# Kernel tuning notes

Hardware: AMD Instinct MI355X
Metric: run time of the kernel (lower is better)

Reference implementation:

```python
import jax, jax.numpy as jnp
import numpy as np

D_MODEL, N_HEADS = 512, 8
HEAD_DIM = D_MODEL // N_HEADS
LN_EPS = 1e-5


def setup_inputs() -> dict:
    key = jax.random.key(0)
    ks = jax.random.split(key, 6)
    b, n = 8, 1024
    x = jax.random.normal(ks[0], (b, n, D_MODEL), dtype=jnp.float32)
    W_qkv = jax.random.normal(ks[1], (D_MODEL, 3 * D_MODEL), dtype=jnp.float32) * (1.0 / np.sqrt(D_MODEL))
    b_qkv = jnp.zeros((3 * D_MODEL,), dtype=jnp.float32)
    reattn_w = jax.random.normal(ks[2], (N_HEADS, N_HEADS), dtype=jnp.float32)
    ln_g = jnp.ones((N_HEADS,), dtype=jnp.float32)
    ln_b = jnp.zeros((N_HEADS,), dtype=jnp.float32)
    W_out = jax.random.normal(ks[3], (D_MODEL, D_MODEL), dtype=jnp.float32) * (1.0 / np.sqrt(D_MODEL))
    b_out = jnp.zeros((D_MODEL,), dtype=jnp.float32)
    return {"x": x, "W_qkv": W_qkv, "b_qkv": b_qkv, "reattn_w": reattn_w,
            "ln_g": ln_g, "ln_b": ln_b, "W_out": W_out, "b_out": b_out}


def reference(x, W_qkv, b_qkv, reattn_w, ln_g, ln_b, W_out, b_out):
    b, n, _ = x.shape
    scale = jnp.float32(HEAD_DIM ** -0.5)  # lsa=False -> non-trainable constant
    qkv = x @ W_qkv + b_qkv                                  # (b, n, 3*d_model)
    q, k, v = jnp.split(qkv, 3, axis=-1)
    def to_heads(t):  # b n (h d) -> b h n d
        return t.reshape(b, n, N_HEADS, HEAD_DIM).transpose(0, 2, 1, 3)
    q, k, v = to_heads(q), to_heads(k), to_heads(v)
    scores = jnp.einsum('bhid,bhjd->bhij', q, k) * scale      # (b, h, n, n)
    attn = jax.nn.softmax(scores, axis=-1)
    # cross-head re-attention mix
    attn = jnp.einsum('bhij,hk->bkij', attn, reattn_w)
    # LayerNorm over the head axis (axis=1)
    mu = jnp.mean(attn, axis=1, keepdims=True)
    var = jnp.var(attn, axis=1, keepdims=True)
    attn = (attn - mu) * jax.lax.rsqrt(var + LN_EPS)
    attn = attn * ln_g[None, :, None, None] + ln_b[None, :, None, None]
    out = jnp.einsum('bhij,bhjd->bhid', attn, v)              # (b, h, n, d)
    out = out.transpose(0, 2, 1, 3).reshape(b, n, D_MODEL)    # b n (h d)
    out = out @ W_out + b_out
    return (out, attn)
```

## Files before the change

### kernel.cpp

```cpp
#include <hip/hip_runtime.h>
#include <hip/hip_bf16.h>

#define SCALE_ 0.125f
#define LN_EPS_ 1e-5f

typedef __attribute__((ext_vector_type(8))) short bf16x8;
typedef __attribute__((ext_vector_type(4))) float f32x4;

__device__ __forceinline__ ushort f2b(float f) {
  union { float f; unsigned u; } x; x.f = f;
  unsigned r = x.u + 0x7FFFu + ((x.u >> 16) & 1u);
  return (ushort)(r >> 16);
}
__device__ __forceinline__ unsigned cvtpk(float lo, float hi) {
  union { __hip_bfloat162 h; unsigned u; } x;
  x.h = __float22bfloat162_rn(make_float2(lo, hi));
  return x.u;
}

__device__ __forceinline__ f32x4 mfma16(bf16x8 a, bf16x8 b, f32x4 c) {
  return __builtin_amdgcn_mfma_f32_16x16x32_bf16(a, b, c, 0, 0, 0);
}

__device__ __forceinline__ void bar_lds() {
  asm volatile("s_waitcnt lgkmcnt(0)\n\ts_barrier" ::: "memory");
  __builtin_amdgcn_sched_barrier(0);
}

__global__ __launch_bounds__(256) void cast_transpose(const float* __restrict__ src,
                                                      ushort* __restrict__ dst,
                                                      int R, int C) {
  __shared__ ushort t[64][65];
  const int tid = threadIdx.x;
  const int c0 = blockIdx.x * 64, r0 = blockIdx.y * 64;
  const int lr = tid >> 2, lc = (tid & 3) * 16;
#pragma unroll
  for (int u = 0; u < 4; ++u) {
    float4 v = *(const float4*)&src[(size_t)(r0 + lr) * C + c0 + lc + u * 4];
    t[lc + u * 4 + 0][lr] = f2b(v.x);
    t[lc + u * 4 + 1][lr] = f2b(v.y);
    t[lc + u * 4 + 2][lr] = f2b(v.z);
    t[lc + u * 4 + 3][lr] = f2b(v.w);
  }
  __syncthreads();
#pragma unroll
  for (int u = 0; u < 2; ++u) {
    bf16x8 o;
#pragma unroll
    for (int e = 0; e < 8; ++e) o[e] = (short)t[lr][lc + u * 8 + e];
    *(bf16x8*)&dst[(size_t)(c0 + lr) * R + r0 + lc + u * 8] = o;
  }
}

__global__ __launch_bounds__(256) void qkv_mfma(const float* __restrict__ x,
                                                const ushort* __restrict__ Wt,
                                                const float* __restrict__ bias,
                                                ushort* __restrict__ q,
                                                ushort* __restrict__ k,
                                                ushort* __restrict__ vt) {
  __shared__ ushort A[128][40];
  __shared__ ushort Bs[128][40];
  const int tid = threadIdx.x;
  const int n0 = blockIdx.x * 128;
  const int m0 = blockIdx.y * 128;
  const int lane = tid & 63, wid = tid >> 6;
  const int wr = wid >> 1, wc = wid & 1;
  const int lr = lane & 15, g4 = lane >> 4;
  const int sr = tid >> 1, sco = (tid & 1) * 16;
  f32x4 acc[4][4] = {};
  for (int k0 = 0; k0 < 512; k0 += 32) {
    {
      const float4* xs = (const float4*)&x[(size_t)(m0 + sr) * 512 + k0 + sco];
      float4 v0 = xs[0], v1 = xs[1], v2 = xs[2], v3 = xs[3];
      bf16x8 p0, p1;
      p0[0] = (short)f2b(v0.x); p0[1] = (short)f2b(v0.y);
      p0[2] = (short)f2b(v0.z); p0[3] = (short)f2b(v0.w);
      p0[4] = (short)f2b(v1.x); p0[5] = (short)f2b(v1.y);
      p0[6] = (short)f2b(v1.z); p0[7] = (short)f2b(v1.w);
      p1[0] = (short)f2b(v2.x); p1[1] = (short)f2b(v2.y);
      p1[2] = (short)f2b(v2.z); p1[3] = (short)f2b(v2.w);
      p1[4] = (short)f2b(v3.x); p1[5] = (short)f2b(v3.y);
      p1[6] = (short)f2b(v3.z); p1[7] = (short)f2b(v3.w);
      *(bf16x8*)&A[sr][sco] = p0;
      *(bf16x8*)&A[sr][sco + 8] = p1;
    }
    {
      const bf16x8* wp = (const bf16x8*)&Wt[(size_t)(n0 + sr) * 512 + k0 + sco];
      *(bf16x8*)&Bs[sr][sco] = wp[0];
      *(bf16x8*)&Bs[sr][sco + 8] = wp[1];
    }
    __syncthreads();
    bf16x8 af[4], bf[4];
#pragma unroll
    for (int mr = 0; mr < 4; ++mr) af[mr] = *(bf16x8*)&A[wr * 64 + mr * 16 + lr][g4 * 8];
#pragma unroll
    for (int nr = 0; nr < 4; ++nr) bf[nr] = *(bf16x8*)&Bs[wc * 64 + nr * 16 + lr][g4 * 8];
#pragma unroll
    for (int mr = 0; mr < 4; ++mr)
#pragma unroll
      for (int nr = 0; nr < 4; ++nr) acc[mr][nr] = mfma16(af[mr], bf[nr], acc[mr][nr]);
    __syncthreads();
  }
  const int part = n0 >> 9;
#pragma unroll
  for (int mr = 0; mr < 4; ++mr)
#pragma unroll
    for (int nr = 0; nr < 4; ++nr) {
      const int n = n0 + wc * 64 + nr * 16 + lr;
      const int h = (n & 511) >> 6, d = n & 63;
      const float bb = bias[n];
#pragma unroll
      for (int r = 0; r < 4; ++r) {
        int token = m0 + wr * 64 + mr * 16 + g4 * 4 + r;
        int bi = token >> 10, ii = token & 1023;
        ushort valb = f2b(acc[mr][nr][r] + bb);
        if (part == 0)
          q[(((size_t)(bi * 8 + h) * 1024 + ii) * 64) + d] = valb;
        else if (part == 1)
          k[(((size_t)(bi * 8 + h) * 1024 + ii) * 64) + d] = valb;
        else
          vt[((size_t)(bi * 8 + h) * 64 + d) * 1024 + ii] = valb;
      }
    }
}

__global__ __launch_bounds__(64) void denoms(const ushort* __restrict__ q,
                                             const ushort* __restrict__ k,
                                             float* __restrict__ invg) {
  const int bid = blockIdx.x;
  const int obid = ((bid & 7) << 8) + (bid >> 3);
  const int bh = obid >> 5;
  const int it = obid & 31;
  const int lane = threadIdx.x;
  const int lr = lane & 15, g4 = lane >> 4;
  const ushort* qh = q + ((size_t)bh * 1024 + it * 32) * 64;
  const ushort* kh = k + (size_t)bh * 65536;

  bf16x8 qf[2][2];
#pragma unroll
  for (int ir = 0; ir < 2; ++ir)
#pragma unroll
    for (int ks = 0; ks < 2; ++ks)
      qf[ir][ks] = *(const bf16x8*)&qh[(size_t)(ir * 16 + lr) * 64 + ks * 32 + g4 * 8];

  float psum[2] = {0.f, 0.f};
  bf16x8 kc[4], kn[4];
#pragma unroll
  for (int jr = 0; jr < 2; ++jr)
#pragma unroll
    for (int ks = 0; ks < 2; ++ks)
      kc[jr * 2 + ks] = *(const bf16x8*)&kh[(size_t)(jr * 16 + lr) * 64 + ks * 32 + g4 * 8];
  for (int jt = 0; jt < 32; ++jt) {
    const int j0n = ((jt + 1) & 31) * 32;
#pragma unroll
    for (int jr = 0; jr < 2; ++jr)
#pragma unroll
      for (int ks = 0; ks < 2; ++ks)
        kn[jr * 2 + ks] =
            *(const bf16x8*)&kh[(size_t)(j0n + jr * 16 + lr) * 64 + ks * 32 + g4 * 8];
    f32x4 sa[2][2] = {};
#pragma unroll
    for (int jr = 0; jr < 2; ++jr)
#pragma unroll
      for (int ir = 0; ir < 2; ++ir) {
        sa[jr][ir] = mfma16(kc[jr * 2 + 0], qf[ir][0], sa[jr][ir]);
        sa[jr][ir] = mfma16(kc[jr * 2 + 1], qf[ir][1], sa[jr][ir]);
      }
#pragma unroll
    for (int jr = 0; jr < 2; ++jr)
#pragma unroll
      for (int ir = 0; ir < 2; ++ir)
#pragma unroll
        for (int r = 0; r < 4; ++r) psum[ir] += __expf(sa[jr][ir][r] * SCALE_);
#pragma unroll
    for (int i = 0; i < 4; ++i) kc[i] = kn[i];
  }
#pragma unroll
  for (int ir = 0; ir < 2; ++ir) {
    float s = psum[ir];
    s += __shfl_xor(s, 16);
    s += __shfl_xor(s, 32);
    psum[ir] = s;
  }
  if (lane < 16) {
    invg[(size_t)bh * 1024 + it * 32 + lr] = 1.0f / psum[0];
    invg[(size_t)bh * 1024 + it * 32 + 16 + lr] = 1.0f / psum[1];
  }
}

__global__ __launch_bounds__(512, 2) void attn_fused(const ushort* __restrict__ q,
                                                     const ushort* __restrict__ k,
                                                     const ushort* __restrict__ vt,
                                                     const float* __restrict__ rw,
                                                     const float* __restrict__ ln_g,
                                                     const float* __restrict__ ln_b,
                                                     const float* __restrict__ invg,
                                                     float* __restrict__ attn,
                                                     ushort* __restrict__ pv) {
  __shared__ float PM[8][32][36];
  __shared__ float wsh[64];
  __shared__ float gsh[8], bsh[8];

  const int tid = threadIdx.x;
  const int lane = tid & 63;
  const int h = tid >> 6;
  const int obid = ((blockIdx.x & 7) << 5) + (blockIdx.x >> 3);
  const int i0 = (obid & 31) * 32;
  const int b = obid >> 5;
  const int lr = lane & 15, g4 = lane >> 4;

  const int bh = b * 8 + h;
  const ushort* qh = q + ((size_t)bh * 1024 + i0) * 64;
  const ushort* kh = k + (size_t)bh * 65536;
  const ushort* vth = vt + (size_t)bh * 65536;

  if (tid < 64) wsh[tid] = rw[tid];
  if (tid < 8) { gsh[tid] = ln_g[tid]; bsh[tid] = ln_b[tid]; }

  bf16x8 qf[2][2];
#pragma unroll
  for (int ir = 0; ir < 2; ++ir)
#pragma unroll
    for (int ks = 0; ks < 2; ++ks)
      qf[ir][ks] = *(const bf16x8*)&qh[(size_t)(ir * 16 + lr) * 64 + ks * 32 + g4 * 8];

  float inv_[2];
#pragma unroll
  for (int ir = 0; ir < 2; ++ir)
    inv_[ir] = invg[(size_t)bh * 1024 + i0 + ir * 16 + lr];

  f32x4 oaccT[4][2] = {};
  const int pair = tid & 1, chunk = tid >> 1;
  const int m_ii = chunk >> 3, m_jj = (chunk & 7) * 4;
  const int k2base = pair * 4;

  bf16x8 kc[4], kn[4];
#pragma unroll
  for (int jr = 0; jr < 2; ++jr)
#pragma unroll
    for (int ks = 0; ks < 2; ++ks)
      kc[jr * 2 + ks] = *(const bf16x8*)&kh[(size_t)(jr * 16 + lr) * 64 + ks * 32 + g4 * 8];

  for (int jt = 0; jt < 32; ++jt) {
    const int j0 = jt * 32;
    const int j0n = ((jt + 1) & 31) * 32;
#pragma unroll
    for (int jr = 0; jr < 2; ++jr)
#pragma unroll
      for (int ks = 0; ks < 2; ++ks)
        kn[jr * 2 + ks] =
            *(const bf16x8*)&kh[(size_t)(j0n + jr * 16 + lr) * 64 + ks * 32 + g4 * 8];

    f32x4 sa[2][2] = {};
#pragma unroll
    for (int jr = 0; jr < 2; ++jr)
#pragma unroll
      for (int ir = 0; ir < 2; ++ir) {
        sa[jr][ir] = mfma16(kc[jr * 2 + 0], qf[ir][0], sa[jr][ir]);
        sa[jr][ir] = mfma16(kc[jr * 2 + 1], qf[ir][1], sa[jr][ir]);
      }
#pragma unroll
    for (int jr = 0; jr < 2; ++jr)
#pragma unroll
      for (int ir = 0; ir < 2; ++ir) {
        f32x4 pw;
#pragma unroll
        for (int r = 0; r < 4; ++r) pw[r] = __expf(sa[jr][ir][r] * SCALE_) * inv_[ir];
        *(f32x4*)&PM[h][ir * 16 + lr][jr * 16 + g4 * 4] = pw;
      }

    bf16x8 vc[4];
#pragma unroll
    for (int dr = 0; dr < 4; ++dr)
      vc[dr] = *(const bf16x8*)&vth[(size_t)(dr * 16 + lr) * 1024 + j0 + g4 * 8];

    bar_lds();

    float4 ph[8];
#pragma unroll
    for (int h2 = 0; h2 < 8; ++h2) ph[h2] = *(const float4*)&PM[h2][m_ii][m_jj];
    float mixed[4][4];
#pragma unroll
    for (int k2l = 0; k2l < 4; ++k2l) {
      float a0 = 0.f, a1 = 0.f, a2 = 0.f, a3 = 0.f;
#pragma unroll
      for (int h2 = 0; h2 < 8; ++h2) {
        float w = wsh[h2 * 8 + k2base + k2l];
        a0 += ph[h2].x * w; a1 += ph[h2].y * w;
        a2 += ph[h2].z * w; a3 += ph[h2].w * w;
      }
      mixed[k2l][0] = a0; mixed[k2l][1] = a1; mixed[k2l][2] = a2; mixed[k2l][3] = a3;
    }
    float mu[4], rs_[4];
#pragma unroll
    for (int e = 0; e < 4; ++e) {
      float mp = mixed[0][e] + mixed[1][e] + mixed[2][e] + mixed[3][e];
      mu[e] = (mp + __shfl_xor(mp, 1)) * 0.125f;
    }
#pragma unroll
    for (int e = 0; e < 4; ++e) {
      float vp = 0.f;
#pragma unroll
      for (int k2l = 0; k2l < 4; ++k2l) {
        float d = mixed[k2l][e] - mu[e];
        vp += d * d;
      }
      float var = (vp + __shfl_xor(vp, 1)) * 0.125f;
      rs_[e] = rsqrtf(var + LN_EPS_);
    }
#pragma unroll
    for (int k2l = 0; k2l < 4; ++k2l) {
      int k2 = k2base + k2l;
      float g = gsh[k2], be = bsh[k2];
      f32x4 o;
      o[0] = (mixed[k2l][0] - mu[0]) * rs_[0] * g + be;
      o[1] = (mixed[k2l][1] - mu[1]) * rs_[1] * g + be;
      o[2] = (mixed[k2l][2] - mu[2]) * rs_[2] * g + be;
      o[3] = (mixed[k2l][3] - mu[3]) * rs_[3] * g + be;
      *(f32x4*)&attn[((size_t)(b * 8 + k2) << 20) + ((size_t)(i0 + m_ii) << 10) +
                     j0 + m_jj] = o;
      *(f32x4*)&PM[k2][m_ii][m_jj] = o;
    }

    bar_lds();

    bf16x8 pab[2];
#pragma unroll
    for (int ic = 0; ic < 2; ++ic) {
      const float* pr = &PM[h][ic * 16 + lr][g4 * 8];
      float4 p0 = *(const float4*)&pr[0];
      float4 p1 = *(const float4*)&pr[4];
      union { bf16x8 v; unsigned u[4]; } pk;
      pk.u[0] = cvtpk(p0.x, p0.y);
      pk.u[1] = cvtpk(p0.z, p0.w);
      pk.u[2] = cvtpk(p1.x, p1.y);
      pk.u[3] = cvtpk(p1.z, p1.w);
      pab[ic] = pk.v;
    }
#pragma unroll
    for (int dr = 0; dr < 4; ++dr) {
      oaccT[dr][0] = mfma16(vc[dr], pab[0], oaccT[dr][0]);
      oaccT[dr][1] = mfma16(vc[dr], pab[1], oaccT[dr][1]);
    }

#pragma unroll
    for (int i = 0; i < 4; ++i) kc[i] = kn[i];
  }

  ushort* po = pv + ((size_t)bh * 1024 + i0) * 64;
#pragma unroll
  for (int ic = 0; ic < 2; ++ic)
#pragma unroll
    for (int dr = 0; dr < 4; ++dr) {
      union { ushort4 s; unsigned u[2]; } o;
      o.u[0] = cvtpk(oaccT[dr][ic][0], oaccT[dr][ic][1]);
      o.u[1] = cvtpk(oaccT[dr][ic][2], oaccT[dr][ic][3]);
      *(ushort4*)&po[(size_t)(ic * 16 + lr) * 64 + dr * 16 + g4 * 4] = o.s;
    }
}

__global__ __launch_bounds__(256) void out_mfma(const ushort* __restrict__ pvb,
                                                const ushort* __restrict__ Wt,
                                                const float* __restrict__ bias,
                                                float* __restrict__ out) {
  __shared__ ushort A[128][40];
  __shared__ ushort Bs[128][40];
  const int tid = threadIdx.x;
  const int n0 = blockIdx.x * 128;
  const int m0 = blockIdx.y * 128;
  const int lane = tid & 63, wid = tid >> 6;
  const int wr = wid >> 1, wc = wid & 1;
  const int lr = lane & 15, g4 = lane >> 4;
  const int sr = tid >> 1, sco = (tid & 1) * 16;
  f32x4 acc[4][4] = {};
  for (int k0 = 0; k0 < 512; k0 += 32) {
    {
      int token = m0 + sr;
      int bi = token >> 10, ii = token & 1023;
      int f = k0 + sco;
      int hh = f >> 6, d = f & 63;
      const bf16x8* src =
          (const bf16x8*)&pvb[(((size_t)(bi * 8 + hh)) * 1024 + ii) * 64 + d];
      *(bf16x8*)&A[sr][sco] = src[0];
      *(bf16x8*)&A[sr][sco + 8] = src[1];
    }
    {
      const bf16x8* wp = (const bf16x8*)&Wt[(size_t)(n0 + sr) * 512 + k0 + sco];
      *(bf16x8*)&Bs[sr][sco] = wp[0];
      *(bf16x8*)&Bs[sr][sco + 8] = wp[1];
    }
    __syncthreads();
    bf16x8 af[4], bf[4];
#pragma unroll
    for (int mr = 0; mr < 4; ++mr) af[mr] = *(bf16x8*)&A[wr * 64 + mr * 16 + lr][g4 * 8];
#pragma unroll
    for (int nr = 0; nr < 4; ++nr) bf[nr] = *(bf16x8*)&Bs[wc * 64 + nr * 16 + lr][g4 * 8];
#pragma unroll
    for (int mr = 0; mr < 4; ++mr)
#pragma unroll
      for (int nr = 0; nr < 4; ++nr) acc[mr][nr] = mfma16(af[mr], bf[nr], acc[mr][nr]);
    __syncthreads();
  }
#pragma unroll
  for (int mr = 0; mr < 4; ++mr)
#pragma unroll
    for (int nr = 0; nr < 4; ++nr) {
      const int n = n0 + wc * 64 + nr * 16 + lr;
      const float bb = bias[n];
#pragma unroll
      for (int r = 0; r < 4; ++r) {
        int token = m0 + wr * 64 + mr * 16 + g4 * 4 + r;
        out[(size_t)token * 512 + n] = acc[mr][nr][r] + bb;
      }
    }
}

extern "C" void kernel_launch(void* const* d_in, const int* in_sizes, int n_in,
                              void* d_out, int out_size, void* d_ws, size_t ws_size,
                              hipStream_t stream) {
  const float* x    = (const float*)d_in[0];
  const float* Wqkv = (const float*)d_in[1];
  const float* bqkv = (const float*)d_in[2];
  const float* rw   = (const float*)d_in[3];
  const float* lng  = (const float*)d_in[4];
  const float* lnb  = (const float*)d_in[5];
  const float* Wout = (const float*)d_in[6];
  const float* bout = (const float*)d_in[7];

  float* out  = (float*)d_out;
  float* attn = (float*)d_out + 4194304;

  char* wsb = (char*)d_ws;
  ushort* q     = (ushort*)(wsb);
  ushort* k     = (ushort*)(wsb + (8u << 20));
  ushort* vt    = (ushort*)(wsb + (16u << 20));
  ushort* pvb   = (ushort*)(wsb + (24u << 20));
  ushort* Wqkvt = (ushort*)(wsb + (32u << 20));
  ushort* Woutt = (ushort*)(wsb + (33u << 20) + (1u << 19));
  float*  invg  = (float*)(wsb + (34u << 20));

  cast_transpose<<<dim3(24, 8), 256, 0, stream>>>(Wqkv, Wqkvt, 512, 1536);
  cast_transpose<<<dim3(8, 8), 256, 0, stream>>>(Wout, Woutt, 512, 512);

  qkv_mfma<<<dim3(12, 64), 256, 0, stream>>>(x, Wqkvt, bqkv, q, k, vt);
  denoms<<<dim3(2048), 64, 0, stream>>>(q, k, invg);
  attn_fused<<<dim3(256), 512, 0, stream>>>(q, k, vt, rw, lng, lnb, invg, attn, pvb);
  out_mfma<<<dim3(4, 64), 256, 0, stream>>>(pvb, Woutt, bout, out);
}
```

Measured before the change: 190.1 us.

## Add dedicated store warps with double-buffered LDS for attn output writes

```diff
diff --git a/kernel.cpp b/kernel.cpp
--- a/kernel.cpp
+++ b/kernel.cpp
@@ -188,7 +188,7 @@
   }
 }
 
-__global__ __launch_bounds__(512, 2) void attn_fused(const ushort* __restrict__ q,
+__global__ __launch_bounds__(768, 2) void attn_fused(const ushort* __restrict__ q,
                                                      const ushort* __restrict__ k,
                                                      const ushort* __restrict__ vt,
                                                      const float* __restrict__ rw,
@@ -197,20 +197,21 @@
                                                      const float* __restrict__ invg,
                                                      float* __restrict__ attn,
                                                      ushort* __restrict__ pv) {
-  __shared__ float PM[8][32][36];
+  __shared__ float PM[2][8][32][36];
   __shared__ float wsh[64];
   __shared__ float gsh[8], bsh[8];
 
   const int tid = threadIdx.x;
   const int lane = tid & 63;
-  const int h = tid >> 6;
+  const int wid = tid >> 6;
+  const bool is_compute = wid < 8;
+  const int h = wid & 7;
   const int obid = ((blockIdx.x & 7) << 5) + (blockIdx.x >> 3);
   const int i0 = (obid & 31) * 32;
   const int b = obid >> 5;
   const int lr = lane & 15, g4 = lane >> 4;
 
   const int bh = b * 8 + h;
-  const ushort* qh = q + ((size_t)bh * 1024 + i0) * 64;
   const ushort* kh = k + (size_t)bh * 65536;
   const ushort* vth = vt + (size_t)bh * 65536;
 
@@ -218,145 +219,152 @@
   if (tid < 8) { gsh[tid] = ln_g[tid]; bsh[tid] = ln_b[tid]; }
 
   bf16x8 qf[2][2];
-#pragma unroll
-  for (int ir = 0; ir < 2; ++ir)
-#pragma unroll
-    for (int ks = 0; ks < 2; ++ks)
-      qf[ir][ks] = *(const bf16x8*)&qh[(size_t)(ir * 16 + lr) * 64 + ks * 32 + g4 * 8];
-
   float inv_[2];
-#pragma unroll
-  for (int ir = 0; ir < 2; ++ir)
-    inv_[ir] = invg[(size_t)bh * 1024 + i0 + ir * 16 + lr];
+  if (is_compute) {
+    const ushort* qh = q + ((size_t)bh * 1024 + i0) * 64;
+#pragma unroll
+    for (int ir = 0; ir < 2; ++ir)
+#pragma unroll
+      for (int ks = 0; ks < 2; ++ks)
+        qf[ir][ks] = *(const bf16x8*)&qh[(size_t)(ir * 16 + lr) * 64 + ks * 32 + g4 * 8];
+#pragma unroll
+    for (int ir = 0; ir < 2; ++ir)
+      inv_[ir] = invg[(size_t)bh * 1024 + i0 + ir * 16 + lr];
+  }
 
   f32x4 oaccT[4][2] = {};
   const int pair = tid & 1, chunk = tid >> 1;
-  const int m_ii = chunk >> 3, m_jj = (chunk & 7) * 4;
+  const int m_ii = (chunk >> 3) & 31, m_jj = (chunk & 7) * 4;
   const int k2base = pair * 4;
-
-  bf16x8 kc[4], kn[4];
-#pragma unroll
-  for (int jr = 0; jr < 2; ++jr)
-#pragma unroll
-    for (int ks = 0; ks < 2; ++ks)
-      kc[jr * 2 + ks] = *(const bf16x8*)&kh[(size_t)(jr * 16 + lr) * 64 + ks * 32 + g4 * 8];
+  const int st = tid - 512;
+  const int s_ii = st >> 3, s_jj4 = (st & 7) * 4;
 
   for (int jt = 0; jt < 32; ++jt) {
     const int j0 = jt * 32;
-    const int j0n = ((jt + 1) & 31) * 32;
-#pragma unroll
-    for (int jr = 0; jr < 2; ++jr)
-#pragma unroll
-      for (int ks = 0; ks < 2; ++ks)
-        kn[jr * 2 + ks] =
-            *(const bf16x8*)&kh[(size_t)(j0n + jr * 16 + lr) * 64 + ks * 32 + g4 * 8];
-
-    f32x4 sa[2][2] = {};
-#pragma unroll
-    for (int jr = 0; jr < 2; ++jr)
-#pragma unroll
-      for (int ir = 0; ir < 2; ++ir) {
-        sa[jr][ir] = mfma16(kc[jr * 2 + 0], qf[ir][0], sa[jr][ir]);
-        sa[jr][ir] = mfma16(kc[jr * 2 + 1], qf[ir][1], sa[jr][ir]);
-      }
-#pragma unroll
-    for (int jr = 0; jr < 2; ++jr)
-#pragma unroll
-      for (int ir = 0; ir < 2; ++ir) {
-        f32x4 pw;
-#pragma unroll
-        for (int r = 0; r < 4; ++r) pw[r] = __expf(sa[jr][ir][r] * SCALE_) * inv_[ir];
-        *(f32x4*)&PM[h][ir * 16 + lr][jr * 16 + g4 * 4] = pw;
-      }
-
+    const int buf = jt & 1;
     bf16x8 vc[4];
-#pragma unroll
-    for (int dr = 0; dr < 4; ++dr)
-      vc[dr] = *(const bf16x8*)&vth[(size_t)(dr * 16 + lr) * 1024 + j0 + g4 * 8];
+    if (is_compute) {
+      bf16x8 kc[4];
+#pragma unroll
+      for (int jr = 0; jr < 2; ++jr)
+#pragma unroll
+        for (int ks = 0; ks < 2; ++ks)
+          kc[jr * 2 + ks] =
+              *(const bf16x8*)&kh[(size_t)(j0 + jr * 16 + lr) * 64 + ks * 32 + g4 * 8];
+
+      f32x4 sa[2][2] = {};
+#pragma unroll
+      for (int jr = 0; jr < 2; ++jr)
+#pragma unroll
+        for (int ir = 0; ir < 2; ++ir) {
+          sa[jr][ir] = mfma16(kc[jr * 2 + 0], qf[ir][0], sa[jr][ir]);
+          sa[jr][ir] = mfma16(kc[jr * 2 + 1], qf[ir][1], sa[jr][ir]);
+        }
+#pragma unroll
+      for (int jr = 0; jr < 2; ++jr)
+#pragma unroll
+        for (int ir = 0; ir < 2; ++ir) {
+          f32x4 pw;
+#pragma unroll
+          for (int r = 0; r < 4; ++r) pw[r] = __expf(sa[jr][ir][r] * SCALE_) * inv_[ir];
+          *(f32x4*)&PM[buf][h][ir * 16 + lr][jr * 16 + g4 * 4] = pw;
+        }
+#pragma unroll
+      for (int dr = 0; dr < 4; ++dr)
+        vc[dr] = *(const bf16x8*)&vth[(size_t)(dr * 16 + lr) * 1024 + j0 + g4 * 8];
+    }
 
     bar_lds();
 
-    float4 ph[8];
-#pragma unroll
-    for (int h2 = 0; h2 < 8; ++h2) ph[h2] = *(const float4*)&PM[h2][m_ii][m_jj];
-    float mixed[4][4];
-#pragma unroll
-    for (int k2l = 0; k2l < 4; ++k2l) {
-      float a0 = 0.f, a1 = 0.f, a2 = 0.f, a3 = 0.f;
-#pragma unroll
-      for (int h2 = 0; h2 < 8; ++h2) {
-        float w = wsh[h2 * 8 + k2base + k2l];
-        a0 += ph[h2].x * w; a1 += ph[h2].y * w;
-        a2 += ph[h2].z * w; a3 += ph[h2].w * w;
-      }
-      mixed[k2l][0] = a0; mixed[k2l][1] = a1; mixed[k2l][2] = a2; mixed[k2l][3] = a3;
-    }
-    float mu[4], rs_[4];
-#pragma unroll
-    for (int e = 0; e < 4; ++e) {
-      float mp = mixed[0][e] + mixed[1][e] + mixed[2][e] + mixed[3][e];
-      mu[e] = (mp + __shfl_xor(mp, 1)) * 0.125f;
-    }
-#pragma unroll
-    for (int e = 0; e < 4; ++e) {
-      float vp = 0.f;
+    if (is_compute) {
+      float4 ph[8];
+#pragma unroll
+      for (int h2 = 0; h2 < 8; ++h2) ph[h2] = *(const float4*)&PM[buf][h2][m_ii][m_jj];
+      float mixed[4][4];
 #pragma unroll
       for (int k2l = 0; k2l < 4; ++k2l) {
-        float d = mixed[k2l][e] - mu[e];
-        vp += d * d;
-      }
-      float var = (vp + __shfl_xor(vp, 1)) * 0.125f;
-      rs_[e] = rsqrtf(var + LN_EPS_);
-    }
-#pragma unroll
-    for (int k2l = 0; k2l < 4; ++k2l) {
-      int k2 = k2base + k2l;
-      float g = gsh[k2], be = bsh[k2];
-      f32x4 o;
-      o[0] = (mixed[k2l][0] - mu[0]) * rs_[0] * g + be;
-      o[1] = (mixed[k2l][1] - mu[1]) * rs_[1] * g + be;
-      o[2] = (mixed[k2l][2] - mu[2]) * rs_[2] * g + be;
-      o[3] = (mixed[k2l][3] - mu[3]) * rs_[3] * g + be;
-      *(f32x4*)&attn[((size_t)(b * 8 + k2) << 20) + ((size_t)(i0 + m_ii) << 10) +
-                     j0 + m_jj] = o;
-      *(f32x4*)&PM[k2][m_ii][m_jj] = o;
+        float a0 = 0.f, a1 = 0.f, a2 = 0.f, a3 = 0.f;
+#pragma unroll
+        for (int h2 = 0; h2 < 8; ++h2) {
+          float w = wsh[h2 * 8 + k2base + k2l];
+          a0 += ph[h2].x * w; a1 += ph[h2].y * w;
+          a2 += ph[h2].z * w; a3 += ph[h2].w * w;
+        }
+        mixed[k2l][0] = a0; mixed[k2l][1] = a1; mixed[k2l][2] = a2; mixed[k2l][3] = a3;
+      }
+      float mu[4], rs_[4];
+#pragma unroll
+      for (int e = 0; e < 4; ++e) {
+        float mp = mixed[0][e] + mixed[1][e] + mixed[2][e] + mixed[3][e];
+        mu[e] = (mp + __shfl_xor(mp, 1)) * 0.125f;
+      }
+#pragma unroll
+      for (int e = 0; e < 4; ++e) {
+        float vp = 0.f;
+#pragma unroll
+        for (int k2l = 0; k2l < 4; ++k2l) {
+          float d = mixed[k2l][e] - mu[e];
+          vp += d * d;
+        }
+        float var = (vp + __shfl_xor(vp, 1)) * 0.125f;
+        rs_[e] = rsqrtf(var + LN_EPS_);
+      }
+#pragma unroll
+      for (int k2l = 0; k2l < 4; ++k2l) {
+        int k2 = k2base + k2l;
+        float g = gsh[k2], be = bsh[k2];
+        f32x4 o;
+        o[0] = (mixed[k2l][0] - mu[0]) * rs_[0] * g + be;
+        o[1] = (mixed[k2l][1] - mu[1]) * rs_[1] * g + be;
+        o[2] = (mixed[k2l][2] - mu[2]) * rs_[2] * g + be;
+        o[3] = (mixed[k2l][3] - mu[3]) * rs_[3] * g + be;
+        *(f32x4*)&PM[buf][k2][m_ii][m_jj] = o;
+      }
     }
 
     bar_lds();
 
-    bf16x8 pab[2];
-#pragma unroll
-    for (int ic = 0; ic < 2; ++ic) {
-      const float* pr = &PM[h][ic * 16 + lr][g4 * 8];
-      float4 p0 = *(const float4*)&pr[0];
-      float4 p1 = *(const float4*)&pr[4];
-      union { bf16x8 v; unsigned u[4]; } pk;
-      pk.u[0] = cvtpk(p0.x, p0.y);
-      pk.u[1] = cvtpk(p0.z, p0.w);
-      pk.u[2] = cvtpk(p1.x, p1.y);
-      pk.u[3] = cvtpk(p1.z, p1.w);
-      pab[ic] = pk.v;
-    }
-#pragma unroll
-    for (int dr = 0; dr < 4; ++dr) {
-      oaccT[dr][0] = mfma16(vc[dr], pab[0], oaccT[dr][0]);
-      oaccT[dr][1] = mfma16(vc[dr], pab[1], oaccT[dr][1]);
-    }
-
-#pragma unroll
-    for (int i = 0; i < 4; ++i) kc[i] = kn[i];
-  }
-
-  ushort* po = pv + ((size_t)bh * 1024 + i0) * 64;
-#pragma unroll
-  for (int ic = 0; ic < 2; ++ic)
-#pragma unroll
-    for (int dr = 0; dr < 4; ++dr) {
-      union { ushort4 s; unsigned u[2]; } o;
-      o.u[0] = cvtpk(oaccT[dr][ic][0], oaccT[dr][ic][1]);
-      o.u[1] = cvtpk(oaccT[dr][ic][2], oaccT[dr][ic][3]);
-      *(ushort4*)&po[(size_t)(ic * 16 + lr) * 64 + dr * 16 + g4 * 4] = o.s;
-    }
+    if (is_compute) {
+      bf16x8 pab[2];
+#pragma unroll
+      for (int ic = 0; ic < 2; ++ic) {
+        const float* pr = &PM[buf][h][ic * 16 + lr][g4 * 8];
+        float4 p0 = *(const float4*)&pr[0];
+        float4 p1 = *(const float4*)&pr[4];
+        union { bf16x8 v; unsigned u[4]; } pk;
+        pk.u[0] = cvtpk(p0.x, p0.y);
+        pk.u[1] = cvtpk(p0.z, p0.w);
+        pk.u[2] = cvtpk(p1.x, p1.y);
+        pk.u[3] = cvtpk(p1.z, p1.w);
+        pab[ic] = pk.v;
+      }
+#pragma unroll
+      for (int dr = 0; dr < 4; ++dr) {
+        oaccT[dr][0] = mfma16(vc[dr], pab[0], oaccT[dr][0]);
+        oaccT[dr][1] = mfma16(vc[dr], pab[1], oaccT[dr][1]);
+      }
+    } else {
+#pragma unroll
+      for (int k2 = 0; k2 < 8; ++k2) {
+        f32x4 o = *(const f32x4*)&PM[buf][k2][s_ii][s_jj4];
+        *(f32x4*)&attn[((size_t)(b * 8 + k2) << 20) + ((size_t)(i0 + s_ii) << 10) +
+                       j0 + s_jj4] = o;
+      }
+    }
+  }
+
+  if (is_compute) {
+    ushort* po = pv + ((size_t)bh * 1024 + i0) * 64;
+#pragma unroll
+    for (int ic = 0; ic < 2; ++ic)
+#pragma unroll
+      for (int dr = 0; dr < 4; ++dr) {
+        union { ushort4 s; unsigned u[2]; } o;
+        o.u[0] = cvtpk(oaccT[dr][ic][0], oaccT[dr][ic][1]);
+        o.u[1] = cvtpk(oaccT[dr][ic][2], oaccT[dr][ic][3]);
+        *(ushort4*)&po[(size_t)(ic * 16 + lr) * 64 + dr * 16 + g4 * 4] = o.s;
+      }
+  }
 }
 
 __global__ __launch_bounds__(256) void out_mfma(const ushort* __restrict__ pvb,
@@ -444,6 +452,6 @@
 
   qkv_mfma<<<dim3(12, 64), 256, 0, stream>>>(x, Wqkvt, bqkv, q, k, vt);
   denoms<<<dim3(2048), 64, 0, stream>>>(q, k, invg);
-  attn_fused<<<dim3(256), 512, 0, stream>>>(q, k, vt, rw, lng, lnb, invg, attn, pvb);
+  attn_fused<<<dim3(256), 768, 0, stream>>>(q, k, vt, rw, lng, lnb, invg, attn, pvb);
   out_mfma<<<dim3(4, 64), 256, 0, stream>>>(pvb, Woutt, bout, out);
 }
```

Result: slower. 227.2 us (+19.5%).
